# Kernel tuning notes

Measured on AMD Instinct MI355X. Metric: run time of the kernel, lower is better.

## Reference

```python
import jax, jax.numpy as jnp
import numpy as np

B, L, INP, HID, NCLS = 512, 256, 300, 256, 5  # trees, leaves/tree, embed dim, hidden, classes


def setup_inputs() -> dict:
    key = jax.random.key(0)
    ks = jax.random.split(key, 7)
    s_in = 1.0 / np.sqrt(INP).astype(np.float32)
    s_h = 1.0 / np.sqrt(HID).astype(np.float32)
    # W_leaf order: [inp_gate, out_gate, upd_gate]
    # W_nl order:  [inp_ln, inp_rn, fo_l_l, fo_l_r, fo_r_l, fo_r_r, out_ln, out_rn, upd_ln, upd_rn]
    return {
        "embeddings": jax.random.normal(ks[0], (B, L, INP), jnp.float32),
        "W_leaf": jax.random.uniform(ks[1], (3, INP, HID), jnp.float32, -s_in, s_in),
        "b_leaf": jax.random.uniform(ks[2], (3, HID), jnp.float32, -s_in, s_in),
        "W_nl": jax.random.uniform(ks[3], (10, HID, HID), jnp.float32, -s_h, s_h),
        "b_nl": jax.random.uniform(ks[4], (10, HID), jnp.float32, -s_h, s_h),
        "W_out": jax.random.uniform(ks[5], (HID, NCLS), jnp.float32, -s_h, s_h),
        "b_out": jax.random.uniform(ks[6], (NCLS,), jnp.float32, -s_h, s_h),
    }


def reference(embeddings, W_leaf, b_leaf, W_nl, b_nl, W_out, b_out):
    sig, tanh = jax.nn.sigmoid, jnp.tanh
    # ---- leaf nodes (depth 0), batched over all B*L leaves ----
    pre = jnp.einsum('bli,gih->blgh', embeddings, W_leaf) + b_leaf  # [B,L,3,H]
    i_g = sig(pre[:, :, 0])
    o_g = sig(pre[:, :, 1])
    u_g = tanh(pre[:, :, 2])
    c = i_g * u_g                      # [B,L,H]
    h = o_g * sig(c)                   # note: leaf uses sigmoid(cell), as in torch code
    logits = [jnp.einsum('bnh,hc->bnc', h, W_out) + b_out]
    # ---- internal nodes, level-synchronous ----
    Wl = W_nl[0::2]                    # [5,H,H] acting on left hidden
    Wr = W_nl[1::2]                    # [5,H,H] acting on right hidden
    bb = b_nl[0::2] + b_nl[1::2]       # [5,H]
    n = L
    while n > 1:
        lc, rc = c[:, 0::2], c[:, 1::2]
        lh, rh = h[:, 0::2], h[:, 1::2]
        pre = (jnp.einsum('bnh,ghk->bngk', lh, Wl)
               + jnp.einsum('bnh,ghk->bngk', rh, Wr) + bb)  # [B,n/2,5,H]
        inp_g = sig(pre[:, :, 0])
        fol_g = sig(pre[:, :, 1])
        for_g = sig(pre[:, :, 2])
        out_g = sig(pre[:, :, 3])
        upd_g = tanh(pre[:, :, 4])
        c = inp_g * upd_g + fol_g * lc + for_g * rc
        h = out_g * tanh(c)
        logits.append(jnp.einsum('bnh,hc->bnc', h, W_out) + b_out)
        n //= 2
    # per-node class scores for all 2L-1 nodes (leaves first, root last)
    return jnp.concatenate(logits, axis=1)  # [B, 2L-1, NCLS]
```

## Files before the change

kernel.cpp:

```cpp
#include <hip/hip_runtime.h>
#include <hip/hip_bf16.h>


#define HID 256

typedef __attribute__((ext_vector_type(8))) short short8;
typedef __attribute__((ext_vector_type(4))) float f32x4;
typedef __attribute__((ext_vector_type(4))) unsigned short ushort4v;

__device__ __forceinline__ float rcpf(float x) { return __builtin_amdgcn_rcpf(x); }
__device__ __forceinline__ float sigf(float x) { return rcpf(1.0f + __expf(-x)); }
__device__ __forceinline__ float tanhf_(float x) { return 2.0f * rcpf(1.0f + __expf(-2.0f * x)) - 1.0f; }
__device__ __forceinline__ unsigned short f2bf(float f) {
    __hip_bfloat16 b = __float2bfloat16(f);
    return *(unsigned short*)&b;
}
__device__ __forceinline__ void gload_lds16(const void* g, void* l) {
    __builtin_amdgcn_global_load_lds(
        (const __attribute__((address_space(1))) unsigned int*)g,
        (__attribute__((address_space(3))) unsigned int*)l, 16, 0, 0);
}

template <int NG, int CS, int K, bool LEAF>
__global__ __launch_bounds__(256, 2) void gemm_gates(
    const unsigned short* __restrict__ A,
    const unsigned short* __restrict__ BT,
    const float* __restrict__ bias,
    const float* __restrict__ cprev,
    float* __restrict__ cout,
    unsigned short* __restrict__ hout,
    const float* __restrict__ W_out,
    float* __restrict__ out,
    int log2n, int off)
{
    constexpr int BN  = NG * CS;
    constexpr int NK  = K / 64;
    constexpr int NF  = CS / 32;
    constexpr int NBW = BN / 32;
    constexpr int BUF = (128 + BN) * 128;

    __shared__ char smem[2 * BUF];

    const int t = threadIdx.x;
    const int lane = t & 63;
    const int w = t >> 6;
    const int wm = w >> 1, wn = w & 1;
    const int row0 = blockIdx.x * 128;
    const int cb = blockIdx.y;

    const int l3 = lane >> 3;
    const unsigned int swsrc = (unsigned int)(((lane & 7) ^ l3) * 16);
    unsigned int a_src[4];
    unsigned int b_src[NBW];
#pragma unroll
    for (int q = 0; q < 4; ++q)
        a_src[q] = (unsigned int)(row0 + (w * 4 + q) * 8 + l3) * (K * 2) + swsrc;
#pragma unroll
    for (int q = 0; q < NBW; ++q)
        b_src[q] = (unsigned int)(cb * BN + (w * NBW + q) * 8 + l3) * (K * 2) + swsrc;

    const int swz0 = ((lane >> 4) ^ (lane & 7)) * 16;
    const int swz1 = (((lane >> 4) + 4) ^ (lane & 7)) * 16;
    const int aoff = (wm * 64 + (lane & 15)) * 128;
    const int boff = (wn * (CS / 2) + (lane & 15)) * 128;

    f32x4 acc[4][NG * NF] = {};

    auto STAGE = [&](int buf, int kt) {
        char* As = smem + buf * BUF;
        char* Bs = As + 128 * 128;
        const unsigned int k0b = (unsigned int)kt * 128;
#pragma unroll
        for (int q = 0; q < 4; ++q)
            gload_lds16((const char*)A + (size_t)(a_src[q] + k0b),
                        As + (w * 4 + q) * 1024);
#pragma unroll
        for (int q = 0; q < NBW; ++q)
            gload_lds16((const char*)BT + (size_t)(b_src[q] + k0b),
                        Bs + (w * NBW + q) * 1024);
    };

    STAGE(0, 0);
    asm volatile("s_waitcnt vmcnt(0)" ::: "memory");
    __builtin_amdgcn_s_barrier();

#pragma unroll
    for (int kt = 0; kt < NK; ++kt) {
        const int cur = kt & 1;
        if (kt + 1 < NK) STAGE(cur ^ 1, kt + 1);
        const char* As = smem + cur * BUF;
        const char* Bs = As + 128 * 128;
#pragma unroll
        for (int ks = 0; ks < 2; ++ks) {
            const int sw = ks ? swz1 : swz0;
            short8 a[4];
#pragma unroll
            for (int mf = 0; mf < 4; ++mf)
                a[mf] = *(const short8*)(As + aoff + mf * 2048 + sw);
#pragma unroll
            for (int g = 0; g < NG; ++g)
#pragma unroll
                for (int fc = 0; fc < NF; ++fc) {
                    short8 b = *(const short8*)(Bs + g * (CS * 128) + boff +
                                                fc * 2048 + sw);
#pragma unroll
                    for (int mf = 0; mf < 4; ++mf)
                        acc[mf][g * NF + fc] = __builtin_amdgcn_mfma_f32_16x16x32_bf16(
                            a[mf], b, acc[mf][g * NF + fc], 0, 0, 0);
                }
        }
        asm volatile("s_waitcnt vmcnt(0)" ::: "memory");
        __builtin_amdgcn_s_barrier();
    }

    float* hs = (float*)smem;
    float* Ws = (float*)(smem + 128 * (CS + 1) * 4);
    for (int i = t; i < CS * 5; i += 256) Ws[i] = W_out[cb * CS * 5 + i];

#pragma unroll
    for (int mf = 0; mf < 4; ++mf) {
#pragma unroll
        for (int j = 0; j < 4; ++j) {
            const int rl = wm * 64 + mf * 16 + ((lane >> 4) << 2) + j;
            const int r = row0 + rl;
#pragma unroll
            for (int fc = 0; fc < NF; ++fc) {
                const int cl = wn * (CS / 2) + fc * 16 + (lane & 15);
                const int c = cb * CS + cl;
                float cv, hv;
                if constexpr (LEAF) {
                    float p0 = acc[mf][0 * NF + fc][j] + bias[c];
                    float p1 = acc[mf][1 * NF + fc][j] + bias[256 + c];
                    float p2 = acc[mf][2 * NF + fc][j] + bias[512 + c];
                    cv = sigf(p0) * tanhf_(p2);
                    hv = sigf(p1) * sigf(cv);
                } else {
                    float p0 = acc[mf][0 * NF + fc][j] + bias[c];
                    float p1 = acc[mf][1 * NF + fc][j] + bias[256 + c];
                    float p2 = acc[mf][2 * NF + fc][j] + bias[512 + c];
                    float p3 = acc[mf][3 * NF + fc][j] + bias[768 + c];
                    float p4 = acc[mf][4 * NF + fc][j] + bias[1024 + c];
                    float lc = cprev[(size_t)r * 512 + c];
                    float rc = cprev[(size_t)r * 512 + 256 + c];
                    cv = sigf(p0) * tanhf_(p4) + sigf(p1) * lc + sigf(p2) * rc;
                    hv = sigf(p3) * tanhf_(cv);
                }
                cout[(size_t)r * 256 + c] = cv;
                hout[(size_t)r * 256 + c] = f2bf(hv);
                hs[rl * (CS + 1) + cl] = hv;
            }
        }
    }
    __syncthreads();

    const int nmask = (1 << log2n) - 1;
    for (int idx = t; idx < 128 * 5; idx += 256) {
        int rl = idx / 5, cls = idx - rl * 5;
        float s = 0.f;
#pragma unroll
        for (int c2 = 0; c2 < CS; ++c2)
            s = fmaf(hs[rl * (CS + 1) + c2], Ws[c2 * 5 + cls], s);
        int rg = row0 + rl;
        int b = rg >> log2n, jj = rg & nmask;
        atomicAdd(out + ((size_t)b * 511 + off + jj) * 5 + cls, s);
    }
}

__global__ __launch_bounds__(256) void prep_weights(
    const float* __restrict__ W_leaf, const float* __restrict__ W_nl,
    const float* __restrict__ b_nl, const float* __restrict__ b_out,
    unsigned short* __restrict__ BleafT, unsigned short* __restrict__ BlevT,
    float* __restrict__ bb, float* __restrict__ out)
{
    const int T1 = 768 * 320, T2 = 1280 * 512, T3 = 5 * 256, T4 = 261632 * 5;
    for (int idx = blockIdx.x * 256 + threadIdx.x; idx < T1 + T2 + T3 + T4;
         idx += gridDim.x * 256) {
        if (idx < T1) {
            int colp = idx / 320, k = idx % 320;
            int cbv = colp / 192, rem = colp % 192;
            int g = rem >> 6, cl = rem & 63;
            int c = cbv * 64 + cl;
            float v = (k < 300) ? W_leaf[((size_t)g * 300 + k) * 256 + c] : 0.0f;
            BleafT[(size_t)colp * 320 + k] = f2bf(v);
        } else if (idx < T1 + T2) {
            int i2 = idx - T1;
            int colp = i2 / 512, k = i2 % 512;
            int cb8 = colp / 160, rem = colp % 160;
            int g = rem >> 5, cl = rem & 31;
            int c = cb8 * 32 + cl;
            float v = W_nl[((size_t)(2 * g + (k >= 256)) * 256 + (k & 255)) * 256 + c];
            BlevT[(size_t)colp * 512 + k] = f2bf(v);
        } else if (idx < T1 + T2 + T3) {
            int i3 = idx - T1 - T2;
            bb[i3] = b_nl[(size_t)(i3 >> 8) * 512 + (i3 & 255)] +
                     b_nl[(size_t)(i3 >> 8) * 512 + 256 + (i3 & 255)];
        } else {
            int i4 = idx - T1 - T2 - T3;
            out[i4] = b_out[i4 % 5];
        }
    }
}

__global__ __launch_bounds__(256) void emb_to_bf16(
    const float* __restrict__ emb, unsigned short* __restrict__ embB)
{
    const int total = 131072 * 80;
    for (int idx = blockIdx.x * 256 + threadIdx.x; idx < total;
         idx += gridDim.x * 256) {
        int r = idx / 80, q = idx % 80;
        ushort4v o;
        if (q < 75) {
            const float4 v = *(const float4*)(emb + (size_t)r * 300 + q * 4);
            o.x = f2bf(v.x); o.y = f2bf(v.y); o.z = f2bf(v.z); o.w = f2bf(v.w);
        } else {
            o.x = 0; o.y = 0; o.z = 0; o.w = 0;
        }
        *(ushort4v*)(embB + (size_t)r * 320 + q * 4) = o;
    }
}

extern "C" void kernel_launch(void* const* d_in, const int* in_sizes, int n_in,
                              void* d_out, int out_size, void* d_ws, size_t ws_size,
                              hipStream_t stream) {
    const float* emb    = (const float*)d_in[0];
    const float* W_leaf = (const float*)d_in[1];
    const float* b_leaf = (const float*)d_in[2];
    const float* W_nl   = (const float*)d_in[3];
    const float* b_nl   = (const float*)d_in[4];
    const float* W_out  = (const float*)d_in[5];
    const float* b_out  = (const float*)d_in[6];
    float* out = (float*)d_out;

    char* ws = (char*)d_ws;
    unsigned short* embB   = (unsigned short*)(ws);
    unsigned short* BleafT = (unsigned short*)(ws + 83886080);
    unsigned short* BlevT  = (unsigned short*)(ws + 84377600);
    float*          bb     = (float*)(ws + 85688320);
    float*          cA     = (float*)(ws + 85693440);
    unsigned short* hA     = (unsigned short*)(ws + 219911168);
    float*          cB     = (float*)(ws + 287020032);
    unsigned short* hB     = (unsigned short*)(ws + 354128896);

    prep_weights<<<2048, 256, 0, stream>>>(W_leaf, W_nl, b_nl, b_out,
                                           BleafT, BlevT, bb, out);
    emb_to_bf16<<<2048, 256, 0, stream>>>(emb, embB);

    gemm_gates<3, 64, 320, true><<<dim3(1024, 4), 256, 0, stream>>>(
        embB, BleafT, b_leaf, nullptr, cA, hA, W_out, out, 8, 0);

    const unsigned short* hp = hA;
    const float* cp = cA;
    int off = 256;
    for (int lev = 1; lev <= 8; ++lev) {
        int log2n = 8 - lev;
        int n = 1 << log2n;
        int M = 512 * n;
        float* cd = (lev & 1) ? cB : cA;
        unsigned short* hd = (lev & 1) ? hB : hA;
        gemm_gates<5, 32, 512, false><<<dim3(M / 128, 8), 256, 0, stream>>>(
            hp, BlevT, bb, cp, cd, hd, W_out, out, log2n, off);
        cp = cd;
        hp = hd;
        off += n;
    }
}
```

Measured before the change: 502.3 us.

## Single-buffer B tile and fix column slice at 32 to raise occupancy

The column slice per block is fixed at 32, so the leaf GEMM now uses 8 column blocks instead of 4 with a matching weight repack. The B tile drops from double buffering to a single buffer that is reloaded between two barriers each k-step, while A stays double-buffered. Launch bounds go from 2 to 3 blocks per CU, made possible by the smaller LDS footprint and fewer accumulators. The trade-off is an extra barrier per k-step and B loads that are no longer overlapped with compute, plus A tiles reloaded across twice as many leaf column blocks.

```diff
diff --git a/kernel.cpp b/kernel.cpp
--- a/kernel.cpp
+++ b/kernel.cpp
@@ -21,8 +21,8 @@
         (__attribute__((address_space(3))) unsigned int*)l, 16, 0, 0);
 }
 
-template <int NG, int CS, int K, bool LEAF>
-__global__ __launch_bounds__(256, 2) void gemm_gates(
+template <int NG, int K, bool LEAF>
+__global__ __launch_bounds__(256, 3) void gemm_gates(
     const unsigned short* __restrict__ A,
     const unsigned short* __restrict__ BT,
     const float* __restrict__ bias,
@@ -33,13 +33,14 @@
     float* __restrict__ out,
     int log2n, int off)
 {
+    constexpr int CS  = 32;
     constexpr int BN  = NG * CS;
     constexpr int NK  = K / 64;
-    constexpr int NF  = CS / 32;
     constexpr int NBW = BN / 32;
-    constexpr int BUF = (128 + BN) * 128;
-
-    __shared__ char smem[2 * BUF];
+    constexpr int ABUF = 128 * 128;
+
+    __shared__ char smem[2 * ABUF + BN * 128];
+    char* Bs = smem + 2 * ABUF;
 
     const int t = threadIdx.x;
     const int lane = t & 63;
@@ -62,34 +63,37 @@
     const int swz0 = ((lane >> 4) ^ (lane & 7)) * 16;
     const int swz1 = (((lane >> 4) + 4) ^ (lane & 7)) * 16;
     const int aoff = (wm * 64 + (lane & 15)) * 128;
-    const int boff = (wn * (CS / 2) + (lane & 15)) * 128;
-
-    f32x4 acc[4][NG * NF] = {};
-
-    auto STAGE = [&](int buf, int kt) {
-        char* As = smem + buf * BUF;
-        char* Bs = As + 128 * 128;
+    const int boff = (wn * 16 + (lane & 15)) * 128;
+
+    f32x4 acc[4][NG] = {};
+
+    auto STAGE_A = [&](int buf, int kt) {
+        char* As = smem + buf * ABUF;
         const unsigned int k0b = (unsigned int)kt * 128;
 #pragma unroll
         for (int q = 0; q < 4; ++q)
             gload_lds16((const char*)A + (size_t)(a_src[q] + k0b),
                         As + (w * 4 + q) * 1024);
+    };
+    auto STAGE_B = [&](int kt) {
+        const unsigned int k0b = (unsigned int)kt * 128;
 #pragma unroll
         for (int q = 0; q < NBW; ++q)
             gload_lds16((const char*)BT + (size_t)(b_src[q] + k0b),
                         Bs + (w * NBW + q) * 1024);
     };
 
-    STAGE(0, 0);
+    STAGE_A(0, 0);
+    STAGE_B(0);
     asm volatile("s_waitcnt vmcnt(0)" ::: "memory");
     __builtin_amdgcn_s_barrier();
+    asm volatile("" ::: "memory");
 
 #pragma unroll
     for (int kt = 0; kt < NK; ++kt) {
         const int cur = kt & 1;
-        if (kt + 1 < NK) STAGE(cur ^ 1, kt + 1);
-        const char* As = smem + cur * BUF;
-        const char* Bs = As + 128 * 128;
+        if (kt + 1 < NK) STAGE_A(cur ^ 1, kt + 1);
+        const char* As = smem + cur * ABUF;
 #pragma unroll
         for (int ks = 0; ks < 2; ++ks) {
             const int sw = ks ? swz1 : swz0;
@@ -98,23 +102,27 @@
             for (int mf = 0; mf < 4; ++mf)
                 a[mf] = *(const short8*)(As + aoff + mf * 2048 + sw);
 #pragma unroll
-            for (int g = 0; g < NG; ++g)
-#pragma unroll
-                for (int fc = 0; fc < NF; ++fc) {
-                    short8 b = *(const short8*)(Bs + g * (CS * 128) + boff +
-                                                fc * 2048 + sw);
-#pragma unroll
-                    for (int mf = 0; mf < 4; ++mf)
-                        acc[mf][g * NF + fc] = __builtin_amdgcn_mfma_f32_16x16x32_bf16(
-                            a[mf], b, acc[mf][g * NF + fc], 0, 0, 0);
-                }
-        }
-        asm volatile("s_waitcnt vmcnt(0)" ::: "memory");
+            for (int g = 0; g < NG; ++g) {
+                short8 b = *(const short8*)(Bs + g * (CS * 128) + boff + sw);
+#pragma unroll
+                for (int mf = 0; mf < 4; ++mf)
+                    acc[mf][g] = __builtin_amdgcn_mfma_f32_16x16x32_bf16(
+                        a[mf], b, acc[mf][g], 0, 0, 0);
+            }
+        }
+        asm volatile("" ::: "memory");
         __builtin_amdgcn_s_barrier();
+        asm volatile("" ::: "memory");
+        if (kt + 1 < NK) {
+            STAGE_B(kt + 1);
+            asm volatile("s_waitcnt vmcnt(0)" ::: "memory");
+        }
+        __builtin_amdgcn_s_barrier();
+        asm volatile("" ::: "memory");
     }
 
     float* hs = (float*)smem;
-    float* Ws = (float*)(smem + 128 * (CS + 1) * 4);
+    float* Ws = (float*)(smem + 128 * 33 * 4);
     for (int i = t; i < CS * 5; i += 256) Ws[i] = W_out[cb * CS * 5 + i];
 
 #pragma unroll
@@ -123,32 +131,29 @@
         for (int j = 0; j < 4; ++j) {
             const int rl = wm * 64 + mf * 16 + ((lane >> 4) << 2) + j;
             const int r = row0 + rl;
-#pragma unroll
-            for (int fc = 0; fc < NF; ++fc) {
-                const int cl = wn * (CS / 2) + fc * 16 + (lane & 15);
-                const int c = cb * CS + cl;
-                float cv, hv;
-                if constexpr (LEAF) {
-                    float p0 = acc[mf][0 * NF + fc][j] + bias[c];
-                    float p1 = acc[mf][1 * NF + fc][j] + bias[256 + c];
-                    float p2 = acc[mf][2 * NF + fc][j] + bias[512 + c];
-                    cv = sigf(p0) * tanhf_(p2);
-                    hv = sigf(p1) * sigf(cv);
-                } else {
-                    float p0 = acc[mf][0 * NF + fc][j] + bias[c];
-                    float p1 = acc[mf][1 * NF + fc][j] + bias[256 + c];
-                    float p2 = acc[mf][2 * NF + fc][j] + bias[512 + c];
-                    float p3 = acc[mf][3 * NF + fc][j] + bias[768 + c];
-                    float p4 = acc[mf][4 * NF + fc][j] + bias[1024 + c];
-                    float lc = cprev[(size_t)r * 512 + c];
-                    float rc = cprev[(size_t)r * 512 + 256 + c];
-                    cv = sigf(p0) * tanhf_(p4) + sigf(p1) * lc + sigf(p2) * rc;
-                    hv = sigf(p3) * tanhf_(cv);
-                }
-                cout[(size_t)r * 256 + c] = cv;
-                hout[(size_t)r * 256 + c] = f2bf(hv);
-                hs[rl * (CS + 1) + cl] = hv;
+            const int cl = wn * 16 + (lane & 15);
+            const int c = cb * CS + cl;
+            float cv, hv;
+            if constexpr (LEAF) {
+                float p0 = acc[mf][0][j] + bias[c];
+                float p1 = acc[mf][1][j] + bias[256 + c];
+                float p2 = acc[mf][2][j] + bias[512 + c];
+                cv = sigf(p0) * tanhf_(p2);
+                hv = sigf(p1) * sigf(cv);
+            } else {
+                float p0 = acc[mf][0][j] + bias[c];
+                float p1 = acc[mf][1][j] + bias[256 + c];
+                float p2 = acc[mf][2][j] + bias[512 + c];
+                float p3 = acc[mf][3][j] + bias[768 + c];
+                float p4 = acc[mf][4][j] + bias[1024 + c];
+                float lc = cprev[(size_t)r * 512 + c];
+                float rc = cprev[(size_t)r * 512 + 256 + c];
+                cv = sigf(p0) * tanhf_(p4) + sigf(p1) * lc + sigf(p2) * rc;
+                hv = sigf(p3) * tanhf_(cv);
             }
+            cout[(size_t)r * 256 + c] = cv;
+            hout[(size_t)r * 256 + c] = f2bf(hv);
+            hs[rl * 33 + cl] = hv;
         }
     }
     __syncthreads();
@@ -159,7 +164,7 @@
         float s = 0.f;
 #pragma unroll
         for (int c2 = 0; c2 < CS; ++c2)
-            s = fmaf(hs[rl * (CS + 1) + c2], Ws[c2 * 5 + cls], s);
+            s = fmaf(hs[rl * 33 + c2], Ws[c2 * 5 + cls], s);
         int rg = row0 + rl;
         int b = rg >> log2n, jj = rg & nmask;
         atomicAdd(out + ((size_t)b * 511 + off + jj) * 5 + cls, s);
@@ -177,9 +182,9 @@
          idx += gridDim.x * 256) {
         if (idx < T1) {
             int colp = idx / 320, k = idx % 320;
-            int cbv = colp / 192, rem = colp % 192;
-            int g = rem >> 6, cl = rem & 63;
-            int c = cbv * 64 + cl;
+            int cbv = colp / 96, rem = colp % 96;
+            int g = rem >> 5, cl = rem & 31;
+            int c = cbv * 32 + cl;
             float v = (k < 300) ? W_leaf[((size_t)g * 300 + k) * 256 + c] : 0.0f;
             BleafT[(size_t)colp * 320 + k] = f2bf(v);
         } else if (idx < T1 + T2) {
@@ -245,7 +250,7 @@
                                            BleafT, BlevT, bb, out);
     emb_to_bf16<<<2048, 256, 0, stream>>>(emb, embB);
 
-    gemm_gates<3, 64, 320, true><<<dim3(1024, 4), 256, 0, stream>>>(
+    gemm_gates<3, 320, true><<<dim3(1024, 8), 256, 0, stream>>>(
         embB, BleafT, b_leaf, nullptr, cA, hA, W_out, out, 8, 0);
 
     const unsigned short* hp = hA;
@@ -257,7 +262,7 @@
         int M = 512 * n;
         float* cd = (lev & 1) ? cB : cA;
         unsigned short* hd = (lev & 1) ? hB : hA;
-        gemm_gates<5, 32, 512, false><<<dim3(M / 128, 8), 256, 0, stream>>>(
+        gemm_gates<5, 512, false><<<dim3(M / 128, 8), 256, 0, stream>>>(
             hp, BlevT, bb, cp, cd, hd, W_out, out, log2n, off);
         cp = cd;
         hp = hd;
```

After: 512.5 us. 1.02x slower.
